# Kernel tuning notes

Hardware: AMD Instinct MI355X
Metric: run time of the kernel (lower is better)

The kernel has to match this reference:

```python
import jax, jax.numpy as jnp
import numpy as np

B, S, D = 4, 2048, 2048
NH, NKV = 16, 4
HD = D // NH          # 128
GROUPS = NH // NKV    # 4
ROPE_BASE = 1000000.0


def setup_inputs() -> dict:
    key = jax.random.key(0)
    ks = jax.random.split(key, 8)
    sc = 0.02
    return {
        "x": jax.random.normal(ks[0], (B, S, D), dtype=jnp.float32),
        "wq_w": jax.random.normal(ks[1], (D, D), dtype=jnp.float32) * sc,
        "wq_b": jax.random.normal(ks[2], (D,), dtype=jnp.float32) * sc,
        "wk_w": jax.random.normal(ks[3], (NKV * HD, D), dtype=jnp.float32) * sc,
        "wk_b": jax.random.normal(ks[4], (NKV * HD,), dtype=jnp.float32) * sc,
        "wv_w": jax.random.normal(ks[5], (NKV * HD, D), dtype=jnp.float32) * sc,
        "wv_b": jax.random.normal(ks[6], (NKV * HD,), dtype=jnp.float32) * sc,
        "wo_w": jax.random.normal(ks[7], (D, D), dtype=jnp.float32) * sc,
    }


def _rope_cos_sin(seq_len, head_dim, dtype):
    inv_freq = 1.0 / (ROPE_BASE ** (jnp.arange(0, head_dim, 2, dtype=jnp.float32) / head_dim))
    t = jnp.arange(seq_len, dtype=jnp.float32)
    freqs = jnp.outer(t, inv_freq)              # [S, HD/2]
    emb = jnp.concatenate([freqs, freqs], axis=-1)  # [S, HD]
    return jnp.cos(emb).astype(dtype), jnp.sin(emb).astype(dtype)


def _rotate_half(x):
    half = x.shape[-1] // 2
    return jnp.concatenate([-x[..., half:], x[..., :half]], axis=-1)


def reference(x, wq_w, wq_b, wk_w, wk_b, wv_w, wv_b, wo_w):
    # QKV projections (wq/wk/wv have bias; out_proj does not)
    q = x @ wq_w.T + wq_b                       # [B,S,D]
    k = x @ wk_w.T + wk_b                       # [B,S,NKV*HD]
    v = x @ wv_w.T + wv_b

    q = q.reshape(B, S, NH, HD).transpose(0, 2, 1, 3)    # [B,NH,S,HD]
    k = k.reshape(B, S, NKV, HD).transpose(0, 2, 1, 3)   # [B,NKV,S,HD]
    v = v.reshape(B, S, NKV, HD).transpose(0, 2, 1, 3)

    # GQA: repeat_interleave kv heads to match q heads
    k = jnp.repeat(k, GROUPS, axis=1)                    # [B,NH,S,HD]
    v = jnp.repeat(v, GROUPS, axis=1)

    cos, sin = _rope_cos_sin(S, HD, q.dtype)             # [S,HD]
    q = q * cos + _rotate_half(q) * sin
    k = k * cos + _rotate_half(k) * sin

    scale = 1.0 / np.sqrt(HD)
    scores = jnp.einsum("bhqd,bhkd->bhqk", q, k) * scale
    causal = jnp.tril(jnp.ones((S, S), dtype=bool))
    scores = jnp.where(causal, scores, jnp.finfo(scores.dtype).min)
    probs = jax.nn.softmax(scores, axis=-1)
    ctx = jnp.einsum("bhqk,bhkd->bhqd", probs, v)        # [B,NH,S,HD]

    ctx = ctx.transpose(0, 2, 1, 3).reshape(B, S, D)     # b h s d -> b s (h d)
    return ctx @ wo_w.T                                  # [B,S,D]
```

## Files before the change

### kernel.cpp

```cpp
#include <hip/hip_runtime.h>
#include <cstdint>
#include <cstddef>

#define B_   4
#define S_   2048
#define D_   2048
#define NH_  16
#define NKV_ 4
#define HD_  128

typedef __attribute__((ext_vector_type(8))) short short8;
typedef __attribute__((ext_vector_type(4))) float f32x4;

__device__ __forceinline__ unsigned short f2bf(float f) {
    union { float f; unsigned u; } v{f};
    unsigned r = v.u + 0x7FFF + ((v.u >> 16) & 1);
    return (unsigned short)(r >> 16);
}
__device__ __forceinline__ float bf2f(unsigned short h) {
    union { unsigned u; float f; } v{(unsigned)h << 16};
    return v.f;
}
__device__ __forceinline__ void split1(float f, unsigned short& h, unsigned short& l) {
    h = f2bf(f);
    l = f2bf(f - bf2f(h));
}
__device__ __forceinline__ void unpack8(const unsigned* w, short8& hi, short8& lo) {
    unsigned h[4], l[4];
#pragma unroll
    for (int i = 0; i < 4; ++i) {
        h[i] = (w[2*i] & 0xFFFFu) | (w[2*i+1] << 16);
        l[i] = (w[2*i] >> 16) | (w[2*i+1] & 0xFFFF0000u);
    }
    hi = *(short8*)h; lo = *(short8*)l;
}

__global__ __launch_bounds__(256) void split_bf16_k(
    const float* __restrict__ src, ushort* __restrict__ hi, ushort* __restrict__ lo)
{
    size_t i = ((size_t)blockIdx.x * 256 + threadIdx.x) * 4;
    float4 f = *(const float4*)&src[i];
    ushort4 h, l;
    split1(f.x, h.x, l.x); split1(f.y, h.y, l.y);
    split1(f.z, h.z, l.z); split1(f.w, h.w, l.w);
    *(ushort4*)&hi[i] = h;
    *(ushort4*)&lo[i] = l;
}

__global__ __launch_bounds__(256) void gemm_mfma_split(
    const ushort* __restrict__ Ah, const ushort* __restrict__ Al,
    const ushort* __restrict__ Bh, const ushort* __restrict__ Bl,
    const float* __restrict__ bias, float* __restrict__ C,
    int M, int N, int K)
{
    __shared__ ushort sA[2][128 * 32];
    __shared__ ushort sB[2][128 * 32];

    const int tid  = threadIdx.x;
    const int wave = tid >> 6;
    const int lane = tid & 63;
    const int bm = blockIdx.y * 128;
    const int bn = blockIdx.x * 128;
    const int wm = (wave & 1) * 64;
    const int wn = (wave >> 1) * 64;

    f32x4 acc[4][4];
#pragma unroll
    for (int mt = 0; mt < 4; ++mt)
#pragma unroll
        for (int nt = 0; nt < 4; ++nt) acc[mt][nt] = 0.f;

    const ushort* gbase = (wave == 0) ? Ah : (wave == 1) ? Al : (wave == 2) ? Bh : Bl;
    ushort* sbase = (wave == 0) ? sA[0] : (wave == 1) ? sA[1] : (wave == 2) ? sB[0] : sB[1];
    const int rb   = (wave < 2) ? bm : bn;
    const int lrow = lane >> 2;
    const int lcol = (lane & 3) * 8;

    const int koff = (lane >> 4) * 8;
    const int rsel = lane & 15;

    for (int k0 = 0; k0 < K; k0 += 32) {
        __syncthreads();
        const ushort* g0 = gbase + (size_t)(rb + lrow) * K + k0 + lcol;
#pragma unroll
        for (int i = 0; i < 8; ++i) {
            __builtin_amdgcn_global_load_lds(
                (const __attribute__((address_space(1))) unsigned int*)(g0 + (size_t)i * 16 * K),
                (__attribute__((address_space(3))) unsigned int*)(sbase + i * 512),
                16, 0, 0);
        }
        __syncthreads();

        short8 a_h[4], a_l[4], b_h[4], b_l[4];
#pragma unroll
        for (int t = 0; t < 4; ++t) {
            a_h[t] = *(const short8*)&sA[0][(wm + t * 16 + rsel) * 32 + koff];
            a_l[t] = *(const short8*)&sA[1][(wm + t * 16 + rsel) * 32 + koff];
            b_h[t] = *(const short8*)&sB[0][(wn + t * 16 + rsel) * 32 + koff];
            b_l[t] = *(const short8*)&sB[1][(wn + t * 16 + rsel) * 32 + koff];
        }
#pragma unroll
        for (int mt = 0; mt < 4; ++mt)
#pragma unroll
            for (int nt = 0; nt < 4; ++nt) {
                acc[mt][nt] = __builtin_amdgcn_mfma_f32_16x16x32_bf16(a_h[mt], b_h[nt], acc[mt][nt], 0, 0, 0);
                acc[mt][nt] = __builtin_amdgcn_mfma_f32_16x16x32_bf16(a_h[mt], b_l[nt], acc[mt][nt], 0, 0, 0);
                acc[mt][nt] = __builtin_amdgcn_mfma_f32_16x16x32_bf16(a_l[mt], b_h[nt], acc[mt][nt], 0, 0, 0);
            }
    }

    const int crow0 = bm + wm + (lane >> 4) * 4;
    const int ccol0 = bn + wn + (lane & 15);
#pragma unroll
    for (int nt = 0; nt < 4; ++nt) {
        float bb = bias ? bias[ccol0 + nt * 16] : 0.f;
#pragma unroll
        for (int mt = 0; mt < 4; ++mt)
#pragma unroll
            for (int r = 0; r < 4; ++r)
                C[(size_t)(crow0 + mt * 16 + r) * N + ccol0 + nt * 16] = acc[mt][nt][r] + bb;
    }
}

__global__ __launch_bounds__(256) void rope_split_kernel(
    float* __restrict__ t, int H, float scale, int do_rope)
{
    const int tid = threadIdx.x;
    const int rid = blockIdx.x * 2 + (tid >> 7);
    const int d   = tid & 127;
    size_t fbase = (size_t)rid * 128;
    float val;
    if (do_rope) {
        const int s = (rid / H) & (S_ - 1);
        const int j = d & 63;
        float inv  = 1.0f / powf(1.0e6f, (float)j * (1.0f / 64.0f));
        float fr = (float)s * inv;
        float sn, cs; sincosf(fr, &sn, &cs);
        float x0 = t[fbase + d];
        float xp = t[fbase + (d ^ 64)];
        float rot = (d < 64) ? -xp : xp;
        val = fmaf(x0, cs, rot * sn) * scale;
    } else {
        val = t[fbase + d] * scale;
    }
    __syncthreads();
    unsigned short h, l; split1(val, h, l);
    ushort* us = (ushort*)t;
    us[(size_t)rid * 256 + d]       = h;
    us[(size_t)rid * 256 + 128 + d] = l;
}

__global__ __launch_bounds__(256, 2) void flash_attn_mfma(
    const ushort* __restrict__ Qsp, const ushort* __restrict__ Ksp,
    const ushort* __restrict__ Vsp, ushort* __restrict__ ctx_h,
    ushort* __restrict__ ctx_l)
{
    __shared__ __align__(16) ushort Ks[32][280];
    __shared__ __align__(16) unsigned Vt[128][36];

    const int tid  = threadIdx.x;
    const int wave = tid >> 6;
    const int lane = tid & 63;
    const int l15  = lane & 15;
    const int quad = lane >> 4;
    const int h    = blockIdx.y;
    const int b    = blockIdx.z;
    const int kvh  = h >> 2;

    for (int pass = 0; pass < 2; ++pass) {
        const int xq  = pass ? (15 - (int)blockIdx.x) : (int)blockIdx.x;
        const int q0  = xq * 128;
        const int wq0 = q0 + wave * 32;

        short8 qf[2][4][2];
#pragma unroll
        for (int nf = 0; nf < 2; ++nf)
#pragma unroll
            for (int ks = 0; ks < 4; ++ks) {
                size_t base = (((size_t)b * S_ + wq0 + nf * 16 + l15) * NH_ + h) * 256
                            + ks * 32 + quad * 8;
                qf[nf][ks][0] = *(const short8*)&Qsp[base];
                qf[nf][ks][1] = *(const short8*)&Qsp[base + 128];
            }

        f32x4 O[2][8];
#pragma unroll
        for (int mf = 0; mf < 2; ++mf)
#pragma unroll
            for (int nf = 0; nf < 8; ++nf) O[mf][nf] = 0.f;
        float m_[2] = {-3.0e38f, -3.0e38f};
        float l_[2] = {0.f, 0.f};

        const int ntiles = q0 / 32 + 4;
        for (int t = 0; t < ntiles; ++t) {
            const int k0 = t * 32;
            __syncthreads();

#pragma unroll
            for (int i = 0; i < 4; ++i) {
                int c = tid + i * 256;
                int row = c >> 5, seg = c & 31;
                int prow = ((row & 4) << 2) | ((row >> 3) << 2) | (row & 3);
                const ushort* src = Ksp + (((size_t)b * S_ + k0 + row) * NKV_ + kvh) * 256 + seg * 8;
                ushort* dst = &Ks[prow][seg * 8 + (seg >= 16 ? 16 : 0)];
                *(uint4*)dst = *(const uint4*)src;
            }
            {
                int row = tid & 31, fs = tid >> 5;
                const ushort* src = Vsp + (((size_t)b * S_ + k0 + row) * NKV_ + kvh) * 256 + fs * 16;
#pragma unroll
                for (int hf = 0; hf < 2; ++hf) {
                    uint4 hv = *(const uint4*)(src + hf * 8);
                    uint4 lv = *(const uint4*)(src + 128 + hf * 8);
                    const ushort* hp = (const ushort*)&hv;
                    const ushort* lp = (const ushort*)&lv;
#pragma unroll
                    for (int i = 0; i < 8; ++i)
                        Vt[fs * 16 + hf * 8 + i][row] = (unsigned)hp[i] | ((unsigned)lp[i] << 16);
                }
            }
            __syncthreads();

            f32x4 st[2][2];
#pragma unroll
            for (int nf = 0; nf < 2; ++nf)
#pragma unroll
                for (int mf = 0; mf < 2; ++mf) st[nf][mf] = 0.f;
#pragma unroll
            for (int ks = 0; ks < 4; ++ks) {
                short8 kf_h[2], kf_l[2];
#pragma unroll
                for (int mf = 0; mf < 2; ++mf) {
                    kf_h[mf] = *(const short8*)&Ks[mf * 16 + l15][ks * 32 + quad * 8];
                    kf_l[mf] = *(const short8*)&Ks[mf * 16 + l15][144 + ks * 32 + quad * 8];
                }
#pragma unroll
                for (int nf = 0; nf < 2; ++nf)
#pragma unroll
                    for (int mf = 0; mf < 2; ++mf) {
                        st[nf][mf] = __builtin_amdgcn_mfma_f32_16x16x32_bf16(kf_h[mf], qf[nf][ks][0], st[nf][mf], 0, 0, 0);
                        st[nf][mf] = __builtin_amdgcn_mfma_f32_16x16x32_bf16(kf_h[mf], qf[nf][ks][1], st[nf][mf], 0, 0, 0);
                        st[nf][mf] = __builtin_amdgcn_mfma_f32_16x16x32_bf16(kf_l[mf], qf[nf][ks][0], st[nf][mf], 0, 0, 0);
                    }
            }

            if (k0 + 31 > wq0) {
#pragma unroll
                for (int nf = 0; nf < 2; ++nf)
#pragma unroll
                    for (int mf = 0; mf < 2; ++mf)
#pragma unroll
                        for (int r = 0; r < 4; ++r) {
                            int kg = k0 + quad * 8 + mf * 4 + r;
                            int qg = wq0 + nf * 16 + l15;
                            if (kg > qg) st[nf][mf][r] = -3.0e38f;
                        }
            }

            float alp[2];
#pragma unroll
            for (int nf = 0; nf < 2; ++nf) {
                float rm = -3.0e38f;
#pragma unroll
                for (int mf = 0; mf < 2; ++mf)
#pragma unroll
                    for (int r = 0; r < 4; ++r) rm = fmaxf(rm, st[nf][mf][r]);
                rm = fmaxf(rm, __shfl_xor(rm, 16));
                rm = fmaxf(rm, __shfl_xor(rm, 32));
                float mn = fmaxf(m_[nf], rm);
                float a  = __expf(m_[nf] - mn);
                float rs = 0.f;
#pragma unroll
                for (int mf = 0; mf < 2; ++mf)
#pragma unroll
                    for (int r = 0; r < 4; ++r) {
                        float p = __expf(st[nf][mf][r] - mn);
                        st[nf][mf][r] = p;
                        rs += p;
                    }
                rs += __shfl_xor(rs, 16);
                rs += __shfl_xor(rs, 32);
                l_[nf] = l_[nf] * a + rs;
                m_[nf] = mn;
                alp[nf] = a;
            }

#pragma unroll
            for (int omf = 0; omf < 2; ++omf)
#pragma unroll
                for (int r = 0; r < 4; ++r) {
                    float av = __shfl(alp[omf], (lane & 48) | (quad * 4 + r));
#pragma unroll
                    for (int nf = 0; nf < 8; ++nf) O[omf][nf][r] *= av;
                }

            short8 ph[2], pl[2];
#pragma unroll
            for (int omf = 0; omf < 2; ++omf) {
                unsigned hu[4], lu[4];
#pragma unroll
                for (int mf = 0; mf < 2; ++mf)
#pragma unroll
                    for (int pr = 0; pr < 2; ++pr) {
                        unsigned short ah, al, bh, bl;
                        split1(st[omf][mf][pr * 2],     ah, al);
                        split1(st[omf][mf][pr * 2 + 1], bh, bl);
                        hu[mf * 2 + pr] = (unsigned)ah | ((unsigned)bh << 16);
                        lu[mf * 2 + pr] = (unsigned)al | ((unsigned)bl << 16);
                    }
                ph[omf] = *(short8*)hu;
                pl[omf] = *(short8*)lu;
            }

#pragma unroll
            for (int vnf = 0; vnf < 8; ++vnf) {
                const unsigned* vw = &Vt[vnf * 16 + l15][quad * 8];
                unsigned w[8];
                *(uint4*)w       = *(const uint4*)vw;
                *(uint4*)(w + 4) = *(const uint4*)(vw + 4);
                short8 vh, vl;
                unpack8(w, vh, vl);
#pragma unroll
                for (int omf = 0; omf < 2; ++omf) {
                    O[omf][vnf] = __builtin_amdgcn_mfma_f32_16x16x32_bf16(ph[omf], vh, O[omf][vnf], 0, 0, 0);
                    O[omf][vnf] = __builtin_amdgcn_mfma_f32_16x16x32_bf16(ph[omf], vl, O[omf][vnf], 0, 0, 0);
                    O[omf][vnf] = __builtin_amdgcn_mfma_f32_16x16x32_bf16(pl[omf], vh, O[omf][vnf], 0, 0, 0);
                }
            }
        }

        float li[2] = {1.f / l_[0], 1.f / l_[1]};
#pragma unroll
        for (int omf = 0; omf < 2; ++omf)
#pragma unroll
            for (int r = 0; r < 4; ++r) {
                float il = __shfl(li[omf], (lane & 48) | (quad * 4 + r));
                int qrow = wq0 + omf * 16 + quad * 4 + r;
                size_t rowb = ((size_t)b * S_ + qrow) * (size_t)D_ + h * HD_;
#pragma unroll
                for (int nf = 0; nf < 8; ++nf) {
                    float val = O[omf][nf][r] * il;
                    unsigned short hh, ll; split1(val, hh, ll);
                    int feat = nf * 16 + l15;
                    ctx_h[rowb + feat] = hh;
                    ctx_l[rowb + feat] = ll;
                }
            }
    }
}

extern "C" void kernel_launch(void* const* d_in, const int* in_sizes, int n_in,
                              void* d_out, int out_size, void* d_ws, size_t ws_size,
                              hipStream_t stream)
{
    const float* x    = (const float*)d_in[0];
    const float* wq_w = (const float*)d_in[1];
    const float* wq_b = (const float*)d_in[2];
    const float* wk_w = (const float*)d_in[3];
    const float* wk_b = (const float*)d_in[4];
    const float* wv_w = (const float*)d_in[5];
    const float* wv_b = (const float*)d_in[6];
    const float* wo_w = (const float*)d_in[7];
    float* out = (float*)d_out;

    const int M = B_ * S_;
    const size_t NX   = (size_t)M * D_;
    const size_t NKVE = (size_t)M * NKV_ * HD_;
    const size_t NWQ  = (size_t)D_ * D_;
    const size_t NWK  = (size_t)(NKV_ * HD_) * D_;

    float*  q   = (float*)d_ws;
    float*  k   = q + NX;
    float*  v   = k + NKVE;
    ushort* xh  = (ushort*)(v + NKVE);
    ushort* xl  = xh + NX;
    ushort* wqh = xl + NX;
    ushort* wql = wqh + NWQ;
    ushort* wkh = wql + NWQ;
    ushort* wkl = wkh + NWK;
    ushort* wvh = wkl + NWK;
    ushort* wvl = wvh + NWK;
    ushort* woh = wvl + NWK;
    ushort* wol = woh + NWQ;

    split_bf16_k<<<NX  / 1024, 256, 0, stream>>>(x,    xh,  xl);
    split_bf16_k<<<NWQ / 1024, 256, 0, stream>>>(wq_w, wqh, wql);
    split_bf16_k<<<NWK / 1024, 256, 0, stream>>>(wk_w, wkh, wkl);
    split_bf16_k<<<NWK / 1024, 256, 0, stream>>>(wv_w, wvh, wvl);
    split_bf16_k<<<NWQ / 1024, 256, 0, stream>>>(wo_w, woh, wol);

    gemm_mfma_split<<<dim3(D_/128,         M/128), 256, 0, stream>>>(xh, xl, wqh, wql, wq_b, q, M, D_,       D_);
    gemm_mfma_split<<<dim3((NKV_*HD_)/128, M/128), 256, 0, stream>>>(xh, xl, wkh, wkl, wk_b, k, M, NKV_*HD_, D_);
    gemm_mfma_split<<<dim3((NKV_*HD_)/128, M/128), 256, 0, stream>>>(xh, xl, wvh, wvl, wv_b, v, M, NKV_*HD_, D_);

    rope_split_kernel<<<(M * NH_)  / 2, 256, 0, stream>>>(q, NH_,  0.08838834764831845f, 1);
    rope_split_kernel<<<(M * NKV_) / 2, 256, 0, stream>>>(k, NKV_, 1.0f, 1);
    rope_split_kernel<<<(M * NKV_) / 2, 256, 0, stream>>>(v, NKV_, 1.0f, 0);

    flash_attn_mfma<<<dim3(S_/256, NH_, B_), 256, 0, stream>>>(
        (const ushort*)q, (const ushort*)k, (const ushort*)v, xh, xl);

    gemm_mfma_split<<<dim3(D_/128, M/128), 256, 0, stream>>>(xh, xl, woh, wol, nullptr, out, M, D_, D_);
}
```

Baseline: 1.117 ms.

## Double KV tile to 64 keys with direct global-to-LDS K loads and swizzle

Raises the flash-attention key tile from 32 to 64 rows, which halves the number of loop iterations, barriers and online-softmax rescales per query block. K is now copied straight from global memory into LDS with global_load_lds, using an XOR-swizzled layout in place of padding to avoid bank conflicts. The V transpose is rewritten so each lane handles one key row. The larger tile raises LDS use and register pressure (score accumulators grow to 2x4), which could hurt occupancy under launch_bounds(256,2).

```diff
diff --git a/kernel.cpp b/kernel.cpp
--- a/kernel.cpp
+++ b/kernel.cpp
@@ -155,8 +155,8 @@
     const ushort* __restrict__ Vsp, ushort* __restrict__ ctx_h,
     ushort* __restrict__ ctx_l)
 {
-    __shared__ __align__(16) ushort Ks[32][280];
-    __shared__ __align__(16) unsigned Vt[128][36];
+    __shared__ __align__(16) ushort Ks[64 * 256];
+    __shared__ __align__(16) unsigned Vt[128][68];
 
     const int tid  = threadIdx.x;
     const int wave = tid >> 6;
@@ -167,6 +167,21 @@
     const int b    = blockIdx.z;
     const int kvh  = h >> 2;
 
+    const size_t kvstride = (size_t)NKV_ * 256;
+    const ushort* kbase = Ksp + ((size_t)b * S_ * NKV_ + kvh) * 256;
+
+    int koffl[8];
+#pragma unroll
+    for (int i = 0; i < 8; ++i) {
+        int pr = wave * 16 + i * 2 + (lane >> 5);
+        int u  = (lane & 31) ^ (pr & 7);
+        int r  = (pr & 32) | ((pr & 12) << 1) | ((pr & 16) >> 2) | (pr & 3);
+        koffl[i] = r * 1024 + u * 8;
+    }
+
+    const ushort* vbase = Vsp + ((size_t)b * S_ * NKV_ + kvh) * 256
+                        + (size_t)lane * kvstride + wave * 32;
+
     for (int pass = 0; pass < 2; ++pass) {
         const int xq  = pass ? (15 - (int)blockIdx.x) : (int)blockIdx.x;
         const int q0  = xq * 128;
@@ -191,67 +206,76 @@
         float m_[2] = {-3.0e38f, -3.0e38f};
         float l_[2] = {0.f, 0.f};
 
-        const int ntiles = q0 / 32 + 4;
+        const int ntiles = q0 / 64 + 2;
         for (int t = 0; t < ntiles; ++t) {
-            const int k0 = t * 32;
+            const int k0 = t * 64;
             __syncthreads();
 
-#pragma unroll
-            for (int i = 0; i < 4; ++i) {
-                int c = tid + i * 256;
-                int row = c >> 5, seg = c & 31;
-                int prow = ((row & 4) << 2) | ((row >> 3) << 2) | (row & 3);
-                const ushort* src = Ksp + (((size_t)b * S_ + k0 + row) * NKV_ + kvh) * 256 + seg * 8;
-                ushort* dst = &Ks[prow][seg * 8 + (seg >= 16 ? 16 : 0)];
-                *(uint4*)dst = *(const uint4*)src;
-            }
             {
-                int row = tid & 31, fs = tid >> 5;
-                const ushort* src = Vsp + (((size_t)b * S_ + k0 + row) * NKV_ + kvh) * 256 + fs * 16;
+                const ushort* ksrc = kbase + (size_t)k0 * kvstride;
+                ushort* kdst = Ks + (wave * 16) * 256;
+#pragma unroll
+                for (int i = 0; i < 8; ++i) {
+                    __builtin_amdgcn_global_load_lds(
+                        (const __attribute__((address_space(1))) unsigned int*)(ksrc + koffl[i]),
+                        (__attribute__((address_space(3))) unsigned int*)(kdst + i * 512),
+                        16, 0, 0);
+                }
+            }
+            {
+                const ushort* src = vbase + (size_t)k0 * kvstride;
 #pragma unroll
                 for (int hf = 0; hf < 2; ++hf) {
-                    uint4 hv = *(const uint4*)(src + hf * 8);
-                    uint4 lv = *(const uint4*)(src + 128 + hf * 8);
-                    const ushort* hp = (const ushort*)&hv;
-                    const ushort* lp = (const ushort*)&lv;
-#pragma unroll
-                    for (int i = 0; i < 8; ++i)
-                        Vt[fs * 16 + hf * 8 + i][row] = (unsigned)hp[i] | ((unsigned)lp[i] << 16);
+                    uint4 hv0 = *(const uint4*)(src + hf * 16);
+                    uint4 hv1 = *(const uint4*)(src + hf * 16 + 8);
+                    uint4 lv0 = *(const uint4*)(src + 128 + hf * 16);
+                    uint4 lv1 = *(const uint4*)(src + 128 + hf * 16 + 8);
+                    const ushort* hp0 = (const ushort*)&hv0;
+                    const ushort* hp1 = (const ushort*)&hv1;
+                    const ushort* lp0 = (const ushort*)&lv0;
+                    const ushort* lp1 = (const ushort*)&lv1;
+#pragma unroll
+                    for (int i = 0; i < 8; ++i) {
+                        Vt[wave * 32 + hf * 16 + i][lane]     = (unsigned)hp0[i] | ((unsigned)lp0[i] << 16);
+                        Vt[wave * 32 + hf * 16 + 8 + i][lane] = (unsigned)hp1[i] | ((unsigned)lp1[i] << 16);
+                    }
                 }
             }
             __syncthreads();
 
-            f32x4 st[2][2];
+            f32x4 st[2][4];
 #pragma unroll
             for (int nf = 0; nf < 2; ++nf)
 #pragma unroll
-                for (int mf = 0; mf < 2; ++mf) st[nf][mf] = 0.f;
+                for (int mf = 0; mf < 4; ++mf) st[nf][mf] = 0.f;
 #pragma unroll
             for (int ks = 0; ks < 4; ++ks) {
-                short8 kf_h[2], kf_l[2];
-#pragma unroll
-                for (int mf = 0; mf < 2; ++mf) {
-                    kf_h[mf] = *(const short8*)&Ks[mf * 16 + l15][ks * 32 + quad * 8];
-                    kf_l[mf] = *(const short8*)&Ks[mf * 16 + l15][144 + ks * 32 + quad * 8];
+                short8 kf_h[4], kf_l[4];
+#pragma unroll
+                for (int mf = 0; mf < 4; ++mf) {
+                    int pr = mf * 16 + l15;
+                    int sw = pr & 7;
+                    kf_h[mf] = *(const short8*)&Ks[pr * 256 + (((4 * ks + quad) ^ sw) * 8)];
+                    kf_l[mf] = *(const short8*)&Ks[pr * 256 + (((16 + 4 * ks + quad) ^ sw) * 8)];
                 }
 #pragma unroll
                 for (int nf = 0; nf < 2; ++nf)
 #pragma unroll
-                    for (int mf = 0; mf < 2; ++mf) {
+                    for (int mf = 0; mf < 4; ++mf) {
                         st[nf][mf] = __builtin_amdgcn_mfma_f32_16x16x32_bf16(kf_h[mf], qf[nf][ks][0], st[nf][mf], 0, 0, 0);
                         st[nf][mf] = __builtin_amdgcn_mfma_f32_16x16x32_bf16(kf_h[mf], qf[nf][ks][1], st[nf][mf], 0, 0, 0);
                         st[nf][mf] = __builtin_amdgcn_mfma_f32_16x16x32_bf16(kf_l[mf], qf[nf][ks][0], st[nf][mf], 0, 0, 0);
                     }
             }
 
-            if (k0 + 31 > wq0) {
+            if (k0 + 63 > wq0) {
 #pragma unroll
                 for (int nf = 0; nf < 2; ++nf)
 #pragma unroll
-                    for (int mf = 0; mf < 2; ++mf)
+                    for (int mf = 0; mf < 4; ++mf)
 #pragma unroll
                         for (int r = 0; r < 4; ++r) {
-                            int kg = k0 + quad * 8 + mf * 4 + r;
+                            int kg = k0 + ((mf & 2) << 4) + quad * 8 + ((mf & 1) << 2) + r;
                             int qg = wq0 + nf * 16 + l15;
                             if (kg > qg) st[nf][mf][r] = -3.0e38f;
                         }
@@ -262,7 +286,7 @@
             for (int nf = 0; nf < 2; ++nf) {
                 float rm = -3.0e38f;
 #pragma unroll
-                for (int mf = 0; mf < 2; ++mf)
+                for (int mf = 0; mf < 4; ++mf)
 #pragma unroll
                     for (int r = 0; r < 4; ++r) rm = fmaxf(rm, st[nf][mf][r]);
                 rm = fmaxf(rm, __shfl_xor(rm, 16));
@@ -271,7 +295,7 @@
                 float a  = __expf(m_[nf] - mn);
                 float rs = 0.f;
 #pragma unroll
-                for (int mf = 0; mf < 2; ++mf)
+                for (int mf = 0; mf < 4; ++mf)
 #pragma unroll
                     for (int r = 0; r < 4; ++r) {
                         float p = __expf(st[nf][mf][r] - mn);
@@ -294,39 +318,43 @@
                     for (int nf = 0; nf < 8; ++nf) O[omf][nf][r] *= av;
                 }
 
-            short8 ph[2], pl[2];
-#pragma unroll
-            for (int omf = 0; omf < 2; ++omf) {
-                unsigned hu[4], lu[4];
-#pragma unroll
-                for (int mf = 0; mf < 2; ++mf)
-#pragma unroll
-                    for (int pr = 0; pr < 2; ++pr) {
-                        unsigned short ah, al, bh, bl;
-                        split1(st[omf][mf][pr * 2],     ah, al);
-                        split1(st[omf][mf][pr * 2 + 1], bh, bl);
-                        hu[mf * 2 + pr] = (unsigned)ah | ((unsigned)bh << 16);
-                        lu[mf * 2 + pr] = (unsigned)al | ((unsigned)bl << 16);
+            short8 ph[2][2], pl[2][2];
+#pragma unroll
+            for (int omf = 0; omf < 2; ++omf)
+#pragma unroll
+                for (int c = 0; c < 2; ++c) {
+                    unsigned hu[4], lu[4];
+#pragma unroll
+                    for (int mf_ = 0; mf_ < 2; ++mf_)
+#pragma unroll
+                        for (int pr_ = 0; pr_ < 2; ++pr_) {
+                            unsigned short ah, al, bh, bl;
+                            split1(st[omf][c * 2 + mf_][pr_ * 2],     ah, al);
+                            split1(st[omf][c * 2 + mf_][pr_ * 2 + 1], bh, bl);
+                            hu[mf_ * 2 + pr_] = (unsigned)ah | ((unsigned)bh << 16);
+                            lu[mf_ * 2 + pr_] = (unsigned)al | ((unsigned)bl << 16);
+                        }
+                    ph[omf][c] = *(short8*)hu;
+                    pl[omf][c] = *(short8*)lu;
+                }
+
+#pragma unroll
+            for (int c = 0; c < 2; ++c)
+#pragma unroll
+                for (int vnf = 0; vnf < 8; ++vnf) {
+                    const unsigned* vw = &Vt[vnf * 16 + l15][c * 32 + quad * 8];
+                    unsigned w[8];
+                    *(uint4*)w       = *(const uint4*)vw;
+                    *(uint4*)(w + 4) = *(const uint4*)(vw + 4);
+                    short8 vh, vl;
+                    unpack8(w, vh, vl);
+#pragma unroll
+                    for (int omf = 0; omf < 2; ++omf) {
+                        O[omf][vnf] = __builtin_amdgcn_mfma_f32_16x16x32_bf16(ph[omf][c], vh, O[omf][vnf], 0, 0, 0);
+                        O[omf][vnf] = __builtin_amdgcn_mfma_f32_16x16x32_bf16(ph[omf][c], vl, O[omf][vnf], 0, 0, 0);
+                        O[omf][vnf] = __builtin_amdgcn_mfma_f32_16x16x32_bf16(pl[omf][c], vh, O[omf][vnf], 0, 0, 0);
                     }
-                ph[omf] = *(short8*)hu;
-                pl[omf] = *(short8*)lu;
-            }
-
-#pragma unroll
-            for (int vnf = 0; vnf < 8; ++vnf) {
-                const unsigned* vw = &Vt[vnf * 16 + l15][quad * 8];
-                unsigned w[8];
-                *(uint4*)w       = *(const uint4*)vw;
-                *(uint4*)(w + 4) = *(const uint4*)(vw + 4);
-                short8 vh, vl;
-                unpack8(w, vh, vl);
-#pragma unroll
-                for (int omf = 0; omf < 2; ++omf) {
-                    O[omf][vnf] = __builtin_amdgcn_mfma_f32_16x16x32_bf16(ph[omf], vh, O[omf][vnf], 0, 0, 0);
-                    O[omf][vnf] = __builtin_amdgcn_mfma_f32_16x16x32_bf16(ph[omf], vl, O[omf][vnf], 0, 0, 0);
-                    O[omf][vnf] = __builtin_amdgcn_mfma_f32_16x16x32_bf16(pl[omf], vh, O[omf][vnf], 0, 0, 0);
-                }
-            }
+                }
         }
 
         float li[2] = {1.f / l_[0], 1.f / l_[1]};
```

Result: faster. 1.088 ms (-2.6%).
